# Kernel tuning notes

Hardware: AMD Instinct MI355X
Metric: run time of the kernel (lower is better)

Reference implementation:

```python
import jax, jax.numpy as jnp
import numpy as np

N_QUBITS = 6
N_LAYERS = 3
FEATURE_DIM = 512
ENC_HIDDEN = max(32, N_QUBITS * 4)  # 32
HEAD_HIDDEN = 128
G, T = 54, 24
DIM = 2 ** N_QUBITS  # 64


def _ry_batched(angles):
    # angles: [B] -> batched RY matrices [B, 2, 2] (complex64)
    c = jnp.cos(angles * 0.5)
    s = jnp.sin(angles * 0.5)
    U = jnp.stack([jnp.stack([c, -s], -1), jnp.stack([s, c], -1)], -2)
    return U.astype(jnp.complex64)


def _rot(phi, theta, omega):
    # PennyLane Rot = RZ(omega) RY(theta) RZ(phi); returns [2, 2] complex64
    c = jnp.cos(theta * 0.5).astype(jnp.complex64)
    s = jnp.sin(theta * 0.5).astype(jnp.complex64)
    ep = jnp.exp(-0.5j * (phi + omega).astype(jnp.complex64))  # e^{-i(phi+omega)/2}
    em = jnp.exp(-0.5j * (phi - omega).astype(jnp.complex64))  # e^{-i(phi-omega)/2}
    u00 = ep * c
    u01 = -jnp.conj(em) * s
    u10 = em * s
    u11 = jnp.conj(ep) * c
    return jnp.stack([jnp.stack([u00, u01]), jnp.stack([u10, u11])])


def _apply_1q_batched(state, U, q):
    # state: [B, 2^n]; U: [B, 2, 2] (per-sample gate, e.g. data-encoding RY)
    B = state.shape[0]
    st = state.reshape(B, 2 ** q, 2, -1)
    st = jnp.einsum('bij,bljr->blir', U, st)
    return st.reshape(B, -1)


def _apply_1q(state, U, q):
    # state: [B, 2^n]; U: [2, 2] shared across batch (trainable Rot)
    B = state.shape[0]
    st = state.reshape(B, 2 ** q, 2, -1)
    st = jnp.einsum('ij,bljr->blir', U, st)
    return st.reshape(B, -1)


def _apply_cnot(state, c, t):
    # state: [B, 2^n]; flip target axis where control bit == 1
    B = state.shape[0]
    st = state.reshape((B,) + (2,) * N_QUBITS)
    ax_c, ax_t = 1 + c, 1 + t
    s0 = jnp.take(st, 0, axis=ax_c)
    s1 = jnp.take(st, 1, axis=ax_c)
    s1 = jnp.flip(s1, axis=ax_t if ax_t < ax_c else ax_t - 1)
    st = jnp.stack([s0, s1], axis=ax_c)
    return st.reshape(B, -1)


def _expvals_z(state):
    # <Z_q> for every qubit: [B, n]
    B = state.shape[0]
    probs = (state.real ** 2 + state.imag ** 2).reshape((B,) + (2,) * N_QUBITS)
    outs = []
    for q in range(N_QUBITS):
        axes = tuple(i for i in range(1, N_QUBITS + 1) if i != q + 1)
        p = probs.sum(axes)  # [B, 2]
        outs.append(p[:, 0] - p[:, 1])
    return jnp.stack(outs, -1)


def _circuit(angles, q_weights):
    # angles: [B, n_qubits] float32; q_weights: [L, n, 3]
    B = angles.shape[0]
    state = jnp.zeros((B, DIM), jnp.complex64).at[:, 0].set(1.0)
    for layer in range(N_LAYERS):
        # data_reuploading=True -> re-encode every layer
        for q in range(N_QUBITS):
            state = _apply_1q_batched(state, _ry_batched(angles[:, q]), q)
        for q in range(N_QUBITS):
            w = q_weights[layer, q]
            state = _apply_1q(state, _rot(w[0], w[1], w[2]), q)
        for q in range(0, N_QUBITS - 1, 2):
            state = _apply_cnot(state, q, q + 1)
        for q in range(1, N_QUBITS - 1, 2):
            state = _apply_cnot(state, q, q + 1)
        state = _apply_cnot(state, N_QUBITS - 1, 0)  # n_qubits > 2
    return _expvals_z(state)


def setup_inputs() -> dict:
    key = jax.random.key(0)
    ks = jax.random.split(key, 10)
    B = 32768
    return {
        'x': jax.random.normal(ks[0], (B, FEATURE_DIM), jnp.float32),
        'enc_w1': 0.05 * jax.random.normal(ks[1], (FEATURE_DIM, ENC_HIDDEN), jnp.float32),
        'enc_b1': jnp.zeros((ENC_HIDDEN,), jnp.float32),
        'enc_w2': 0.05 * jax.random.normal(ks[2], (ENC_HIDDEN, N_QUBITS), jnp.float32),
        'enc_b2': jnp.zeros((N_QUBITS,), jnp.float32),
        'q_weights': 0.01 * jax.random.normal(ks[3], (N_LAYERS, N_QUBITS, 3), jnp.float32),
        'head_w1': 0.1 * jax.random.normal(ks[4], (N_QUBITS, HEAD_HIDDEN), jnp.float32),
        'head_b1': jnp.zeros((HEAD_HIDDEN,), jnp.float32),
        'head_w2': 0.05 * jax.random.normal(ks[5], (HEAD_HIDDEN, G * T), jnp.float32),
        'head_b2': jnp.zeros((G * T,), jnp.float32),
    }


def reference(x, enc_w1, enc_b1, enc_w2, enc_b2, q_weights,
              head_w1, head_b1, head_w2, head_b2):
    # classical encoder -> angles [B, n_qubits]
    h = jnp.tanh(x @ enc_w1 + enc_b1)
    angles = h @ enc_w2 + enc_b2
    # batched state-vector PQC simulation
    z = _circuit(angles, q_weights).astype(jnp.float32)  # [B, n_qubits]
    # classical head (dropout is identity in eval)
    g = jax.nn.relu(z @ head_w1 + head_b1)
    logits = g @ head_w2 + head_b2
    return logits.reshape(-1, G, T)
```

## Files before the change

### kernel.cpp

```cpp
#include <hip/hip_runtime.h>

typedef __bf16 bf16x8 __attribute__((ext_vector_type(8)));
typedef float floatx4 __attribute__((ext_vector_type(4)));
typedef unsigned short ushort8 __attribute__((ext_vector_type(8)));

__device__ __forceinline__ unsigned short f2bf(float f) {
    unsigned u = __float_as_uint(f);
    u += 0x7fffu + ((u >> 16) & 1u);
    return (unsigned short)(u >> 16);
}

template <int ST>
__device__ __forceinline__ void apply_local(float* fr, float* fi,
    float m00r, float m00i, float m01r, float m01i,
    float m10r, float m10i, float m11r, float m11i) {
#pragma unroll
    for (int i = 0; i < 8; ++i) {
        if ((i & ST) == 0) {
            int i1 = i + ST;
            float r0 = fr[i], u0 = fi[i], r1 = fr[i1], u1 = fi[i1];
            fr[i]  = m00r * r0 - m00i * u0 + m01r * r1 - m01i * u1;
            fi[i]  = m00r * u0 + m00i * r0 + m01r * u1 + m01i * r1;
            fr[i1] = m10r * r0 - m10i * u0 + m11r * r1 - m11i * u1;
            fi[i1] = m10r * u0 + m10i * r0 + m11r * u1 + m11i * r1;
        }
    }
}

template <int XM>
__device__ __forceinline__ void apply_cross(float* fr, float* fi, bool hi,
    float m00r, float m00i, float m01r, float m01i,
    float m10r, float m10i, float m11r, float m11i) {
    float car = hi ? m10r : m00r, cai = hi ? m10i : m00i;
    float cbr = hi ? m11r : m01r, cbi = hi ? m11i : m01i;
#pragma unroll
    for (int j = 0; j < 8; ++j) {
        float mr = fr[j], mi = fi[j];
        float pr = __shfl_xor(mr, XM);
        float pi = __shfl_xor(mi, XM);
        float a0r = hi ? pr : mr, a0i = hi ? pi : mi;
        float a1r = hi ? mr : pr, a1i = hi ? mi : pi;
        fr[j] = car * a0r - cai * a0i + cbr * a1r - cbi * a1i;
        fi[j] = car * a0i + cai * a0r + cbr * a1i + cbi * a1r;
    }
}

#define SWAP2(a, b) { float _t = fr[a]; fr[a] = fr[b]; fr[b] = _t; \
                      _t = fi[a]; fi[a] = fi[b]; fi[b] = _t; }

__global__ __launch_bounds__(512) void prep_kernel(
    const float* __restrict__ hw2, unsigned short* __restrict__ w2t) {
    int t = blockIdx.x * 512 + threadIdx.x;
    int nn = t >> 4;
    int kc = (t & 15) * 8;
    if (nn < 1296) {
        ushort8 pk;
#pragma unroll
        for (int j = 0; j < 8; ++j) pk[j] = f2bf(hw2[(size_t)(kc + j) * 1296 + nn]);
        *(ushort8*)(w2t + (size_t)nn * 128 + kc) = pk;
    }
}

__global__ __launch_bounds__(512)
__attribute__((amdgpu_waves_per_eu(4, 4)))
void mega_kernel(
    const float* __restrict__ x, const float* __restrict__ w1,
    const float* __restrict__ b1, const float* __restrict__ w2,
    const float* __restrict__ b2, const float* __restrict__ qw,
    const float* __restrict__ hw1, const float* __restrict__ hb1,
    const unsigned short* __restrict__ w2t, const float* __restrict__ hb2,
    float* __restrict__ out) {

    __shared__ float part[8][64][33];
    __shared__ float umat_s[144];

    float (*hsh)[33] = part[0];
    float (*casa)[12] = (float (*)[12])part[1];
    char* gl = (char*)&part[3][0][0];
    int tid = threadIdx.x;

    if (tid < 18) {
        float phi = qw[tid * 3], theta = qw[tid * 3 + 1], omega = qw[tid * 3 + 2];
        float c = cosf(0.5f * theta), s = sinf(0.5f * theta);
        float po = 0.5f * (phi + omega), pm = 0.5f * (phi - omega);
        float epr = cosf(po), epi = -sinf(po);
        float emr = cosf(pm), emi = -sinf(pm);
        float* u = umat_s + tid * 8;
        u[0] = epr * c;  u[1] = epi * c;
        u[2] = -emr * s; u[3] = emi * s;
        u[4] = emr * s;  u[5] = emi * s;
        u[6] = epr * c;  u[7] = -epi * c;
    }

    int lane = tid & 63;
    int wave = tid >> 6;
    int swave = __builtin_amdgcn_readfirstlane(wave);
    size_t row = (size_t)blockIdx.x * 64 + lane;
    const float2* x2 = (const float2*)(x + row * 512 + swave * 64);
    const float* wseg = w1 + swave * 64 * 32;

    float acc[32];
#pragma unroll
    for (int j = 0; j < 32; ++j) acc[j] = 0.f;

#pragma clang loop unroll(disable)
    for (int k2 = 0; k2 < 32; ++k2) {
        float2 xv = x2[k2];
        const float* wr = wseg + k2 * 64;
#pragma unroll
        for (int j = 0; j < 32; ++j) acc[j] = fmaf(wr[j], xv.x, acc[j]);
#pragma unroll
        for (int j = 0; j < 32; ++j) acc[j] = fmaf(wr[32 + j], xv.y, acc[j]);
    }
#pragma unroll
    for (int j = 0; j < 32; ++j) part[wave][lane][j] = acc[j];
    __syncthreads();

    {
        int rl = tid & 63;
        int jg = (tid >> 6) * 4;
#pragma unroll
        for (int jj = 0; jj < 4; ++jj) {
            int j = jg + jj;
            float v = b1[j];
#pragma unroll
            for (int w = 0; w < 8; ++w) v += part[w][rl][j];
            hsh[rl][j] = tanhf(v);
        }
    }
    __syncthreads();

    if (tid < 384) {
        int row_a = tid & 63;
        int q = tid >> 6;
        float a = b2[q];
#pragma unroll
        for (int j = 0; j < 32; ++j) a = fmaf(hsh[row_a][j], w2[j * 6 + q], a);
        a *= 0.5f;
        casa[row_a][q * 2]     = cosf(a);
        casa[row_a][q * 2 + 1] = sinf(a);
    }
    __syncthreads();

    int s8 = lane & 7;
    int p = lane >> 3;
    int samp = wave * 8 + s8;
    bool pb4 = (p & 4) != 0, pb2 = (p & 2) != 0, pb1 = (p & 1) != 0;

    float ca[6], sa[6];
#pragma unroll
    for (int q = 0; q < 6; ++q) { ca[q] = casa[samp][q * 2]; sa[q] = casa[samp][q * 2 + 1]; }

    float fr[8], fi[8];
#pragma unroll
    for (int j = 0; j < 8; ++j) { fr[j] = 0.f; fi[j] = 0.f; }
    fr[0] = (p == 0) ? 1.f : 0.f;

#pragma clang loop unroll(disable)
    for (int layer = 0; layer < 3; ++layer) {
        const float* ub = umat_s + layer * 48;
#define MAT(Q)                                                            \
        const float* u = ub + (Q) * 8;                                    \
        float c = ca[Q], ss = sa[Q];                                      \
        float m00r = u[0] * c + u[2] * ss, m00i = u[1] * c + u[3] * ss;   \
        float m01r = u[2] * c - u[0] * ss, m01i = u[3] * c - u[1] * ss;   \
        float m10r = u[4] * c + u[6] * ss, m10i = u[5] * c + u[7] * ss;   \
        float m11r = u[6] * c - u[4] * ss, m11i = u[7] * c - u[5] * ss;
        { MAT(0) apply_cross<32>(fr, fi, pb4, m00r, m00i, m01r, m01i, m10r, m10i, m11r, m11i); }
        { MAT(1) apply_cross<16>(fr, fi, pb2, m00r, m00i, m01r, m01i, m10r, m10i, m11r, m11i); }
        { MAT(2) apply_cross<8>(fr, fi, pb1, m00r, m00i, m01r, m01i, m10r, m10i, m11r, m11i); }
        { MAT(3) apply_local<4>(fr, fi, m00r, m00i, m01r, m01i, m10r, m10i, m11r, m11i); }
        { MAT(4) apply_local<2>(fr, fi, m00r, m00i, m01r, m01i, m10r, m10i, m11r, m11i); }
        { MAT(5) apply_local<1>(fr, fi, m00r, m00i, m01r, m01i, m10r, m10i, m11r, m11i); }
#undef MAT
#pragma unroll
        for (int j = 0; j < 8; ++j) {
            float pr = __shfl_xor(fr[j], 16);
            float pi = __shfl_xor(fi[j], 16);
            fr[j] = pb4 ? pr : fr[j];
            fi[j] = pb4 ? pi : fi[j];
        }
        {
            float tr[8], ti[8];
#pragma unroll
            for (int j = 0; j < 8; ++j) { tr[j] = fr[j]; ti[j] = fi[j]; }
#pragma unroll
            for (int j = 0; j < 8; ++j) {
                fr[j] = pb1 ? tr[j ^ 4] : tr[j];
                fi[j] = pb1 ? ti[j ^ 4] : ti[j];
            }
        }
        SWAP2(2, 3) SWAP2(6, 7)
#pragma unroll
        for (int j = 0; j < 8; ++j) {
            float pr = __shfl_xor(fr[j], 8);
            float pi = __shfl_xor(fi[j], 8);
            fr[j] = pb2 ? pr : fr[j];
            fi[j] = pb2 ? pi : fi[j];
        }
        SWAP2(4, 6) SWAP2(5, 7)
#pragma unroll
        for (int j = 1; j < 8; j += 2) {
            fr[j] = __shfl_xor(fr[j], 32);
            fi[j] = __shfl_xor(fi[j], 32);
        }
    }

    float zt = 0.f, z3 = 0.f, z4 = 0.f, z5 = 0.f;
#pragma unroll
    for (int j = 0; j < 8; ++j) {
        float pp = fr[j] * fr[j] + fi[j] * fi[j];
        zt += pp;
        z3 += (j & 4) ? -pp : pp;
        z4 += (j & 2) ? -pp : pp;
        z5 += (j & 1) ? -pp : pp;
    }
    float zz[6];
    zz[0] = pb4 ? -zt : zt;
    zz[1] = pb2 ? -zt : zt;
    zz[2] = pb1 ? -zt : zt;
    zz[3] = z3; zz[4] = z4; zz[5] = z5;
#pragma unroll
    for (int q = 0; q < 6; ++q) {
        zz[q] += __shfl_xor(zz[q], 8);
        zz[q] += __shfl_xor(zz[q], 16);
        zz[q] += __shfl_xor(zz[q], 32);
    }

    {
        int a7 = samp & 7;
#pragma unroll
        for (int half = 0; half < 2; ++half) {
            ushort8 pk;
#pragma unroll
            for (int jj = 0; jj < 8; ++jj) {
                int j = p * 16 + half * 8 + jj;
                float a = hb1[j];
#pragma unroll
                for (int q = 0; q < 6; ++q) a = fmaf(zz[q], hw1[q * 128 + j], a);
                a = fmaxf(a, 0.f);
                pk[jj] = f2bf(a);
            }
            int u = (p * 2 + half) ^ a7;
            *(ushort8*)(gl + samp * 256 + u * 16) = pk;
        }
    }
    __syncthreads();

    {
        int l15 = lane & 15, quad = lane >> 4;
        int row0 = blockIdx.x * 64;
        int a7 = l15 & 7;

        for (int n = wave; n < 27; n += 8) {
            int col0 = n * 48;
#pragma unroll
            for (int t = 0; t < 3; ++t) {
                const unsigned short* ap =
                    w2t + (size_t)(col0 + t * 16 + l15) * 128 + quad * 8;

                floatx4 acc4[4];
#pragma unroll
                for (int i = 0; i < 4; ++i) acc4[i] = (floatx4)0.f;

#pragma unroll
                for (int ks = 0; ks < 4; ++ks) {
                    bf16x8 af = *(const bf16x8*)(ap + ks * 32);
                    bf16x8 bf[4];
#pragma unroll
                    for (int sub = 0; sub < 4; ++sub) {
                        int rowg = sub * 16 + l15;
                        int u = (quad + 4 * ks) ^ a7;
                        bf[sub] = *(const bf16x8*)(gl + rowg * 256 + u * 16);
                    }
#pragma unroll
                    for (int sub = 0; sub < 4; ++sub)
                        acc4[sub] = __builtin_amdgcn_mfma_f32_16x16x32_bf16(
                            af, bf[sub], acc4[sub], 0, 0, 0);
                }

                const float* bb = hb2 + col0 + t * 16 + quad * 4;
                floatx4 bias = { bb[0], bb[1], bb[2], bb[3] };
#pragma unroll
                for (int sub = 0; sub < 4; ++sub) {
                    floatx4 v = acc4[sub] + bias;
                    floatx4* dst = (floatx4*)(out +
                        (size_t)(row0 + sub * 16 + l15) * 1296 + col0 + t * 16 + quad * 4);
                    *dst = v;
                }
            }
        }
    }
}

extern "C" void kernel_launch(void* const* d_in, const int* in_sizes, int n_in,
                              void* d_out, int out_size, void* d_ws, size_t ws_size,
                              hipStream_t stream) {
    const float* x   = (const float*)d_in[0];
    const float* ew1 = (const float*)d_in[1];
    const float* eb1 = (const float*)d_in[2];
    const float* ew2 = (const float*)d_in[3];
    const float* eb2 = (const float*)d_in[4];
    const float* qw  = (const float*)d_in[5];
    const float* hw1 = (const float*)d_in[6];
    const float* hb1 = (const float*)d_in[7];
    const float* hw2 = (const float*)d_in[8];
    const float* hb2 = (const float*)d_in[9];
    float* out = (float*)d_out;

    char* ws = (char*)d_ws;
    unsigned short* w2t = (unsigned short*)(ws);

    prep_kernel<<<dim3(41), dim3(512), 0, stream>>>(hw2, w2t);
    mega_kernel<<<dim3(512), dim3(512), 0, stream>>>(
        x, ew1, eb1, ew2, eb2, qw, hw1, hb1, w2t, hb2, out);
}
```

Before: 347.0 us.

## Split fused kernel into front encoder/circuit kernel and separate head GEMM kernel

```diff
diff --git a/kernel.cpp b/kernel.cpp
--- a/kernel.cpp
+++ b/kernel.cpp
@@ -61,22 +61,19 @@
     }
 }
 
-__global__ __launch_bounds__(512)
-__attribute__((amdgpu_waves_per_eu(4, 4)))
-void mega_kernel(
+__global__ __launch_bounds__(512, 4) void front_kernel(
     const float* __restrict__ x, const float* __restrict__ w1,
     const float* __restrict__ b1, const float* __restrict__ w2,
     const float* __restrict__ b2, const float* __restrict__ qw,
     const float* __restrict__ hw1, const float* __restrict__ hb1,
-    const unsigned short* __restrict__ w2t, const float* __restrict__ hb2,
-    float* __restrict__ out) {
+    unsigned short* __restrict__ g) {
 
     __shared__ float part[8][64][33];
     __shared__ float umat_s[144];
 
     float (*hsh)[33] = part[0];
     float (*casa)[12] = (float (*)[12])part[1];
-    char* gl = (char*)&part[3][0][0];
+
     int tid = threadIdx.x;
 
     if (tid < 18) {
@@ -228,7 +225,7 @@
     }
 
     {
-        int a7 = samp & 7;
+        unsigned short* gp = g + ((size_t)blockIdx.x * 64 + samp) * 128 + p * 16;
 #pragma unroll
         for (int half = 0; half < 2; ++half) {
             ushort8 pk;
@@ -241,54 +238,52 @@
                 a = fmaxf(a, 0.f);
                 pk[jj] = f2bf(a);
             }
-            int u = (p * 2 + half) ^ a7;
-            *(ushort8*)(gl + samp * 256 + u * 16) = pk;
-        }
+            *(ushort8*)(gp + half * 8) = pk;
+        }
+    }
+}
+
+__global__ __launch_bounds__(256) void head_gemm(
+    const unsigned short* __restrict__ g, const unsigned short* __restrict__ w2t,
+    const float* __restrict__ b2, float* __restrict__ out) {
+    __shared__ unsigned short gl[16 * 128];
+
+    int tid = threadIdx.x;
+    int row0 = blockIdx.x * 16;
+
+    {
+        int r = tid >> 4;
+        int u = tid & 15;
+        ushort8 v = *(const ushort8*)(g + (size_t)(row0 + r) * 128 + u * 8);
+        int us = u ^ (r & 7);
+        *(ushort8*)(gl + r * 128 + us * 8) = v;
     }
     __syncthreads();
 
-    {
-        int l15 = lane & 15, quad = lane >> 4;
-        int row0 = blockIdx.x * 64;
-        int a7 = l15 & 7;
-
-        for (int n = wave; n < 27; n += 8) {
-            int col0 = n * 48;
-#pragma unroll
-            for (int t = 0; t < 3; ++t) {
-                const unsigned short* ap =
-                    w2t + (size_t)(col0 + t * 16 + l15) * 128 + quad * 8;
-
-                floatx4 acc4[4];
-#pragma unroll
-                for (int i = 0; i < 4; ++i) acc4[i] = (floatx4)0.f;
-
-#pragma unroll
-                for (int ks = 0; ks < 4; ++ks) {
-                    bf16x8 af = *(const bf16x8*)(ap + ks * 32);
-                    bf16x8 bf[4];
-#pragma unroll
-                    for (int sub = 0; sub < 4; ++sub) {
-                        int rowg = sub * 16 + l15;
-                        int u = (quad + 4 * ks) ^ a7;
-                        bf[sub] = *(const bf16x8*)(gl + rowg * 256 + u * 16);
-                    }
-#pragma unroll
-                    for (int sub = 0; sub < 4; ++sub)
-                        acc4[sub] = __builtin_amdgcn_mfma_f32_16x16x32_bf16(
-                            af, bf[sub], acc4[sub], 0, 0, 0);
-                }
-
-                const float* bb = hb2 + col0 + t * 16 + quad * 4;
-                floatx4 bias = { bb[0], bb[1], bb[2], bb[3] };
-#pragma unroll
-                for (int sub = 0; sub < 4; ++sub) {
-                    floatx4 v = acc4[sub] + bias;
-                    floatx4* dst = (floatx4*)(out +
-                        (size_t)(row0 + sub * 16 + l15) * 1296 + col0 + t * 16 + quad * 4);
-                    *dst = v;
-                }
+    int lane = tid & 63, wv = tid >> 6;
+    int l15 = lane & 15, quad = lane >> 4;
+    int a7 = l15 & 7;
+
+    for (int n = wv; n < 27; n += 4) {
+        int col0 = n * 48;
+#pragma unroll
+        for (int t = 0; t < 3; ++t) {
+            const unsigned short* ap =
+                w2t + (size_t)(col0 + t * 16 + l15) * 128 + quad * 8;
+
+            floatx4 acc = (floatx4)0.f;
+#pragma unroll
+            for (int ks = 0; ks < 4; ++ks) {
+                bf16x8 af = *(const bf16x8*)(ap + ks * 32);
+                int u = (quad + 4 * ks) ^ a7;
+                bf16x8 bf = *(const bf16x8*)(gl + l15 * 128 + u * 8);
+                acc = __builtin_amdgcn_mfma_f32_16x16x32_bf16(af, bf, acc, 0, 0, 0);
             }
+
+            const float* bb = b2 + col0 + t * 16 + quad * 4;
+            floatx4 bias = { bb[0], bb[1], bb[2], bb[3] };
+            floatx4 v = acc + bias;
+            *(floatx4*)(out + (size_t)(row0 + l15) * 1296 + col0 + t * 16 + quad * 4) = v;
         }
     }
 }
@@ -309,9 +304,11 @@
     float* out = (float*)d_out;
 
     char* ws = (char*)d_ws;
-    unsigned short* w2t = (unsigned short*)(ws);
+    unsigned short* g   = (unsigned short*)(ws);
+    unsigned short* w2t = (unsigned short*)(ws + 8388608);
 
     prep_kernel<<<dim3(41), dim3(512), 0, stream>>>(hw2, w2t);
-    mega_kernel<<<dim3(512), dim3(512), 0, stream>>>(
-        x, ew1, eb1, ew2, eb2, qw, hw1, hb1, w2t, hb2, out);
-}
+    front_kernel<<<dim3(512), dim3(512), 0, stream>>>(
+        x, ew1, eb1, ew2, eb2, qw, hw1, hb1, g);
+    head_gemm<<<dim3(2048), dim3(256), 0, stream>>>(g, w2t, hb2, out);
+}
```

Result: slower. 370.9 us (+6.9%).
